# Optimization experiments

Measured on AMD Instinct MI355X. Metric: run time of the kernel, lower is better.

## Reference

```python
import jax, jax.numpy as jnp
import numpy as np

NUM_SELECT = 128  # num_select['layer1']


def setup_inputs() -> dict:
    key = jax.random.key(0)
    k1, k2 = jax.random.split(key)
    B, S, C, NC = 32, 4096, 256, 200
    x = jax.random.normal(k1, (B, S, C), dtype=jnp.float32)
    W = jax.random.normal(k2, (C, NC), dtype=jnp.float32) * (1.0 / np.sqrt(C))
    b = jnp.zeros((NC,), dtype=jnp.float32)
    return {"x": x, "W": W, "b": b}


def reference(x, W, b):
    # x: [B, S, C]; classifier logits: [B, S, NC]
    logits = jnp.einsum('bsc,cn->bsn', x, W) + b
    probs = jax.nn.softmax(logits, axis=-1)
    # per-token max class probability -> [B, S]
    max_ids = jnp.max(probs, axis=-1)
    # sort tokens per sample by confidence, descending (vectorized over batch)
    ranks = jnp.argsort(-max_ids, axis=-1)          # [B, S]
    top = ranks[:, :NUM_SELECT]                     # [B, num_select]
    # gather selected token features -> [B, num_select, C]
    selections = jnp.take_along_axis(x, top[:, :, None], axis=1)
    return selections
```

## Files before the change

kernel.cpp:

```cpp
#include <hip/hip_runtime.h>
#include <stdint.h>

#define CDIM 256
#define NCLS 200
#define NSEL 128
#define SEQ  4096
#define RPB  16
#define CCH  32

__device__ __forceinline__ float np_expf(float x) {
    const float LOG2E = 1.442695040888963407359924681001892137f;
    const float MAGIC = 12582912.0f;
    const float CW_HI = -6.93145752e-1f;
    const float CW_LO = -1.42860677e-6f;

    float q = __fsub_rn(__fmaf_rn(x, LOG2E, MAGIC), MAGIC);

    float y = __fmaf_rn(q, CW_HI, x);
    y = __fmaf_rn(q, CW_LO, y);

    float num = __fmaf_rn(5.082762527590693718096e-04f, y,
                          6.757896990527504603057e-03f);
    num = __fmaf_rn(num, y, 5.114512081637298353406e-02f);
    num = __fmaf_rn(num, y, 2.473615434895520810817e-01f);
    num = __fmaf_rn(num, y, 7.257664613233124478488e-01f);
    num = __fmaf_rn(num, y, 9.999999999980870924916e-01f);

    float den = __fmaf_rn(2.159509375685829852307e-02f, y,
                          -2.742335390411667452936e-01f);
    den = __fmaf_rn(den, y, 1.0f);

    const float r = __fdiv_rn(num, den);
    return ldexpf(r, (int)q);
}

__global__ __launch_bounds__(256) void score_kernel(
    const float* __restrict__ x, const float* __restrict__ W,
    const float* __restrict__ bias, float* __restrict__ scores)
{
    __shared__ __align__(16) float xs[RPB * CDIM];
    __shared__ __align__(16) float lg[RPB * NCLS];
    __shared__ float mx[RPB][16];
    __shared__ float sp[RPB][16];
    __shared__ float mrow[RPB];

    const int tid = threadIdx.x;
    const long long row0 = (long long)blockIdx.x * RPB;

    {
        const float4* xg = reinterpret_cast<const float4*>(x + row0 * CDIM);
        float4* xs4 = reinterpret_cast<float4*>(xs);
        for (int i = tid; i < RPB * CDIM / 4; i += 256) xs4[i] = xg[i];
    }
    __syncthreads();

    const int rg = tid / 50;
    const int q  = tid - rg * 50;
    const bool active = (tid < 200);

    float acc[4][4][8];
    #pragma unroll
    for (int r = 0; r < 4; ++r)
        #pragma unroll
        for (int k = 0; k < 4; ++k)
            #pragma unroll
            for (int j = 0; j < 8; ++j) acc[r][k][j] = 0.0f;

    if (active) {
        const float4* Wq = reinterpret_cast<const float4*>(W) + q;
        for (int c8 = 0; c8 < CDIM / CCH; ++c8) {
            const int cc = c8 * CCH;
            #pragma unroll
            for (int i = 3; i >= 0; --i) {
                float4 xq0[4], xq1[4];
                #pragma unroll
                for (int r = 0; r < 4; ++r) {
                    const float* xrow = &xs[(rg * 4 + r) * CDIM + cc + 8 * i];
                    xq0[r] = *reinterpret_cast<const float4*>(xrow);
                    xq1[r] = *reinterpret_cast<const float4*>(xrow + 4);
                }
                #pragma unroll
                for (int j = 0; j < 8; ++j) {
                    const float4 wv = Wq[(long long)(cc + 8 * i + j) * 50];
                    #pragma unroll
                    for (int r = 0; r < 4; ++r) {
                        const float xv = (j < 4)
                            ? reinterpret_cast<const float*>(&xq0[r])[j]
                            : reinterpret_cast<const float*>(&xq1[r])[j - 4];
                        acc[r][0][j] = __fmaf_rn(xv, wv.x, acc[r][0][j]);
                        acc[r][1][j] = __fmaf_rn(xv, wv.y, acc[r][1][j]);
                        acc[r][2][j] = __fmaf_rn(xv, wv.z, acc[r][2][j]);
                        acc[r][3][j] = __fmaf_rn(xv, wv.w, acc[r][3][j]);
                    }
                }
            }
        }

        const float4 bq = reinterpret_cast<const float4*>(bias)[q];
        const float bv[4] = { bq.x, bq.y, bq.z, bq.w };
        #pragma unroll
        for (int r = 0; r < 4; ++r) {
            float h[4];
            #pragma unroll
            for (int k = 0; k < 4; ++k) {
                const float* a = acc[r][k];
                h[k] = __fadd_rn(
                    __fadd_rn(__fadd_rn(a[0], a[1]), __fadd_rn(a[2], a[3])),
                    __fadd_rn(__fadd_rn(a[4], a[5]), __fadd_rn(a[6], a[7])));
                h[k] = __fadd_rn(h[k], bv[k]);
            }
            *reinterpret_cast<float4*>(&lg[(rg * 4 + r) * NCLS + 4 * q]) =
                make_float4(h[0], h[1], h[2], h[3]);
        }
    }
    __syncthreads();

    {
        const int r = tid >> 4, l = tid & 15;
        float mv = lg[r * NCLS + l];
        for (int n = l + 16; n < NCLS; n += 16) mv = fmaxf(mv, lg[r * NCLS + n]);
        mx[r][l] = mv;
    }
    __syncthreads();
    if (tid < RPB) {
        float mv = mx[tid][0];
        #pragma unroll
        for (int l = 1; l < 16; ++l) mv = fmaxf(mv, mx[tid][l]);
        mrow[tid] = mv;
    }
    __syncthreads();

    for (int i = tid; i < RPB * NCLS; i += 256) {
        const int r = i / NCLS;
        lg[i] = np_expf(__fsub_rn(lg[i], mrow[r]));
    }
    __syncthreads();

    {
        const int r = tid >> 4, sub = tid & 15;
        const int k = sub & 7, blk = sub >> 3;
        const float* a = &lg[r * NCLS + (blk ? 96 : 0)];
        const int len = blk ? 104 : 96;
        float c = a[k];
        for (int i = 8; i < len; i += 8) c = __fadd_rn(c, a[i + k]);
        sp[r][blk * 8 + k] = c;
    }
    __syncthreads();

    if (tid < RPB) {
        const float* p = sp[tid];
        const float s1 =
            __fadd_rn(__fadd_rn(__fadd_rn(p[0], p[1]), __fadd_rn(p[2], p[3])),
                      __fadd_rn(__fadd_rn(p[4], p[5]), __fadd_rn(p[6], p[7])));
        const float s2 =
            __fadd_rn(__fadd_rn(__fadd_rn(p[8], p[9]), __fadd_rn(p[10], p[11])),
                      __fadd_rn(__fadd_rn(p[12], p[13]), __fadd_rn(p[14], p[15])));
        const float S = __fadd_rn(s1, s2);
        scores[row0 + tid] = __fdiv_rn(1.0f, S);
    }
}

__global__ __launch_bounds__(256) void sort_gather_kernel(
    const float* __restrict__ pmax, const float* __restrict__ x,
    float* __restrict__ out)
{
    __shared__ uint64_t K[SEQ];

    const int tid = threadIdx.x;
    const int b   = blockIdx.x;

    for (int i = tid; i < SEQ; i += 256) {
        const uint32_t pb = __float_as_uint(pmax[(long long)b * SEQ + i]);
        K[i] = ((uint64_t)pb << 12) | (uint64_t)(SEQ - 1 - i);
    }
    __syncthreads();

    for (int k = 2; k <= SEQ; k <<= 1) {
        for (int j = k >> 1; j > 0; j >>= 1) {
            for (int t = tid; t < SEQ / 2; t += 256) {
                const int i = ((t & ~(j - 1)) << 1) | (t & (j - 1));
                const int p = i | j;
                const bool desc = ((i & k) == 0);
                const uint64_t a = K[i], c = K[p];
                const bool sw = desc ? (a < c) : (a > c);
                if (sw) { K[i] = c; K[p] = a; }
            }
            __syncthreads();
        }
    }

    const float4* x4   = reinterpret_cast<const float4*>(x);
    float4*       out4 = reinterpret_cast<float4*>(out);
    for (int t = tid; t < NSEL * (CDIM / 4); t += 256) {
        const int jj = t >> 6;
        const int c4 = t & 63;
        const int idx = (SEQ - 1) - (int)(K[jj] & (uint64_t)(SEQ - 1));
        out4[((long long)b * NSEL + jj) * (CDIM / 4) + c4] =
            x4[((long long)b * SEQ + idx) * (CDIM / 4) + c4];
    }
}

extern "C" void kernel_launch(void* const* d_in, const int* in_sizes, int n_in,
                              void* d_out, int out_size, void* d_ws, size_t ws_size,
                              hipStream_t stream) {
    const float* x    = (const float*)d_in[0];
    const float* W    = (const float*)d_in[1];
    const float* bias = (const float*)d_in[2];
    float* out   = (float*)d_out;
    float* score = (float*)d_ws;

    const long long nrows = (long long)in_sizes[0] / CDIM;
    const int B = out_size / (NSEL * CDIM);

    score_kernel<<<(int)(nrows / RPB), 256, 0, stream>>>(x, W, bias, score);
    sort_gather_kernel<<<B, 256, 0, stream>>>(score, x, out);
}
```

Baseline: 526.8 us.

## Software-pipeline W loads with register double buffering, wave-aligned GEMM mapping

```diff
diff --git a/kernel.cpp b/kernel.cpp
--- a/kernel.cpp
+++ b/kernel.cpp
@@ -39,12 +39,13 @@
     const float* __restrict__ bias, float* __restrict__ scores)
 {
     __shared__ __align__(16) float xs[RPB * CDIM];
-    __shared__ __align__(16) float lg[RPB * NCLS];
     __shared__ float mx[RPB][16];
     __shared__ float sp[RPB][16];
     __shared__ float mrow[RPB];
 
-    const int tid = threadIdx.x;
+    const int tid  = threadIdx.x;
+    const int wid  = tid >> 6;
+    const int lane = tid & 63;
     const long long row0 = (long long)blockIdx.x * RPB;
 
     {
@@ -54,9 +55,9 @@
     }
     __syncthreads();
 
-    const int rg = tid / 50;
-    const int q  = tid - rg * 50;
-    const bool active = (tid < 200);
+    const int rg = wid;
+    const int q  = (lane < 50) ? lane : 49;
+    const float* Wq = W + 4 * q;
 
     float acc[4][4][8];
     #pragma unroll
@@ -66,36 +67,56 @@
             #pragma unroll
             for (int j = 0; j < 8; ++j) acc[r][k][j] = 0.0f;
 
-    if (active) {
-        const float4* Wq = reinterpret_cast<const float4*>(W) + q;
-        for (int c8 = 0; c8 < CDIM / CCH; ++c8) {
-            const int cc = c8 * CCH;
-            #pragma unroll
-            for (int i = 3; i >= 0; --i) {
-                float4 xq0[4], xq1[4];
-                #pragma unroll
-                for (int r = 0; r < 4; ++r) {
-                    const float* xrow = &xs[(rg * 4 + r) * CDIM + cc + 8 * i];
-                    xq0[r] = *reinterpret_cast<const float4*>(xrow);
-                    xq1[r] = *reinterpret_cast<const float4*>(xrow + 4);
-                }
-                #pragma unroll
-                for (int j = 0; j < 8; ++j) {
-                    const float4 wv = Wq[(long long)(cc + 8 * i + j) * 50];
-                    #pragma unroll
-                    for (int r = 0; r < 4; ++r) {
-                        const float xv = (j < 4)
-                            ? reinterpret_cast<const float*>(&xq0[r])[j]
-                            : reinterpret_cast<const float*>(&xq1[r])[j - 4];
-                        acc[r][0][j] = __fmaf_rn(xv, wv.x, acc[r][0][j]);
-                        acc[r][1][j] = __fmaf_rn(xv, wv.y, acc[r][1][j]);
-                        acc[r][2][j] = __fmaf_rn(xv, wv.z, acc[r][2][j]);
-                        acc[r][3][j] = __fmaf_rn(xv, wv.w, acc[r][3][j]);
-                    }
-                }
-            }
-        }
-
+    float4 bufA[8], bufB[8];
+
+    #pragma unroll
+    for (int j = 0; j < 8; ++j)
+        bufA[j] = *reinterpret_cast<const float4*>(Wq + (24 + j) * NCLS);
+
+#define STEP(I, CUR, NXT, NROW, DOLOAD)                                       \
+    {                                                                         \
+        if (DOLOAD) {                                                         \
+            _Pragma("unroll")                                                 \
+            for (int j = 0; j < 8; ++j)                                       \
+                NXT[j] = *reinterpret_cast<const float4*>(                    \
+                    Wq + (long long)((NROW) + j) * NCLS);                     \
+        }                                                                     \
+        float4 xq0[4], xq1[4];                                                \
+        _Pragma("unroll")                                                     \
+        for (int r = 0; r < 4; ++r) {                                         \
+            const float* xrow = &xs[(rg * 4 + r) * CDIM + cc + 8 * (I)];      \
+            xq0[r] = *reinterpret_cast<const float4*>(xrow);                  \
+            xq1[r] = *reinterpret_cast<const float4*>(xrow + 4);              \
+        }                                                                     \
+        _Pragma("unroll")                                                     \
+        for (int j = 0; j < 8; ++j) {                                         \
+            const float4 wv = CUR[j];                                         \
+            _Pragma("unroll")                                                 \
+            for (int r = 0; r < 4; ++r) {                                     \
+                const float xv = (j < 4)                                      \
+                    ? reinterpret_cast<const float*>(&xq0[r])[j]              \
+                    : reinterpret_cast<const float*>(&xq1[r])[j - 4];         \
+                acc[r][0][j] = __fmaf_rn(xv, wv.x, acc[r][0][j]);             \
+                acc[r][1][j] = __fmaf_rn(xv, wv.y, acc[r][1][j]);             \
+                acc[r][2][j] = __fmaf_rn(xv, wv.z, acc[r][2][j]);             \
+                acc[r][3][j] = __fmaf_rn(xv, wv.w, acc[r][3][j]);             \
+            }                                                                 \
+        }                                                                     \
+    }
+
+    for (int c8 = 0; c8 < CDIM / CCH; ++c8) {
+        const int cc = c8 * CCH;
+        STEP(3, bufA, bufB, cc + 16, true)
+        STEP(2, bufB, bufA, cc + 8,  true)
+        STEP(1, bufA, bufB, cc + 0,  true)
+        STEP(0, bufB, bufA, cc + 32 + 24, (c8 < 7))
+    }
+#undef STEP
+
+    __syncthreads();
+    float* lg = xs;
+
+    if (lane < 50) {
         const float4 bq = reinterpret_cast<const float4*>(bias)[q];
         const float bv[4] = { bq.x, bq.y, bq.z, bq.w };
         #pragma unroll
```

Result: slower. 663.6 us (+26.0%).
